# Kernel tuning notes

Measured on AMD Instinct MI355X. Metric: run time of the kernel, lower is better.

The kernel has to match this reference:

```python
import jax, jax.numpy as jnp
import numpy as np
from jax import lax

B, C, H, W = 32, 512, 56, 56
CO = 512
EPS = 1e-5

def binarize(x):
    # sign binarization with hardtanh straight-through estimator (BNN 1w1a)
    xc = jnp.clip(x, -1.0, 1.0)
    return xc + lax.stop_gradient(jnp.sign(x) - xc)

def batchnorm(y, g, b, m, v):
    # inference-mode BN with running stats, per-channel over NCHW
    inv = g * lax.rsqrt(v + EPS)
    return y * inv[None, :, None, None] + (b - m * inv)[None, :, None, None]

def setup_inputs() -> dict:
    key = jax.random.key(0)
    ks = jax.random.split(key, 11)
    return {
        "x": jax.random.normal(ks[0], (B, C, H, W), dtype=jnp.float32),
        "w_dw": jax.random.normal(ks[1], (C, 1, 3, 3), dtype=jnp.float32),
        "w_pw": jax.random.normal(ks[2], (CO, C, 1, 1), dtype=jnp.float32),
        "g1": jax.random.uniform(ks[3], (C,), dtype=jnp.float32),
        "b1": jax.random.normal(ks[4], (C,), dtype=jnp.float32),
        "m1": jax.random.normal(ks[5], (C,), dtype=jnp.float32),
        "v1": jax.random.uniform(ks[6], (C,), dtype=jnp.float32),
        "g2": jax.random.uniform(ks[7], (CO,), dtype=jnp.float32),
        "b2": jax.random.normal(ks[8], (CO,), dtype=jnp.float32),
        "m2": jax.random.normal(ks[9], (CO,), dtype=jnp.float32),
        "v2": jax.random.uniform(ks[10], (CO,), dtype=jnp.float32),
    }

def reference(x, w_dw, w_pw, g1, b1, m1, v1, g2, b2, m2, v2):
    dn = ('NCHW', 'OIHW', 'NCHW')
    # binary depthwise 3x3, stride 1, pad 1, groups=C
    out = lax.conv_general_dilated(
        binarize(x), binarize(w_dw), window_strides=(1, 1),
        padding=((1, 1), (1, 1)), feature_group_count=C,
        dimension_numbers=dn)
    out = batchnorm(out, g1, b1, m1, v1)
    # binary pointwise 1x1
    out = lax.conv_general_dilated(
        binarize(out), binarize(w_pw), window_strides=(1, 1),
        padding=((0, 0), (0, 0)), dimension_numbers=dn)
    out = batchnorm(out, g2, b2, m2, v2)
    return out
```

## Files before the change

### kernel.cpp

```cpp
#include <hip/hip_runtime.h>

#define BB 32
#define CC 512
#define COO 512
#define HH 56
#define WW 56
#define HW 3136
#define NPOS 100352
#define EPSF 1e-5f

typedef unsigned long long u64;
typedef unsigned int u32;
typedef unsigned short u16;
typedef float f32x4 __attribute__((ext_vector_type(4)));

#define OFF_S1      0
#define OFF_WBITS   6422528
#define OFF_WN      6455296
#define OFF_NT      6455872
#define OFF_BN2INV  6456832
#define OFF_BN2BETA 6458880

__global__ __launch_bounds__(256) void setup_kernel(
    const float* __restrict__ w_dw, const float* __restrict__ w_pw,
    const float* __restrict__ g1, const float* __restrict__ b1,
    const float* __restrict__ m1, const float* __restrict__ v1,
    const float* __restrict__ g2, const float* __restrict__ b2,
    const float* __restrict__ m2, const float* __restrict__ v2,
    u64* __restrict__ wbits, u64* __restrict__ wn, u64* __restrict__ NT,
    float* __restrict__ bn2inv, float* __restrict__ bn2beta) {
    const int t = blockIdx.x * 256 + threadIdx.x;

    {
        int o = t >> 3, wi = t & 7;
        const float* wp = w_pw + (size_t)o * CC + wi * 64;
        u64 wrd = 0;
        #pragma unroll 8
        for (int k = 0; k < 64; ++k)
            wrd |= (u64)(wp[k] >= 0.f) << k;
        wbits[t] = wrd;
    }

    if (t < CC) {
        float i2 = g2[t] / sqrtf(v2[t] + EPSF);
        bn2inv[t]  = i2;
        bn2beta[t] = b2[t] - m2[t] * i2;
    } else if (t >= 512 && t < 584) {
        int q = t - 512, cw = q & 7, tap = q >> 3;
        u64 wv = 0;
        for (int cl = 0; cl < 64; ++cl)
            wv |= (u64)(w_dw[(size_t)(cw * 64 + cl) * 9 + tap] < 0.f) << cl;
        wn[tap * 8 + cw] = wv;
    } else if (t >= 1024 && t < 1048) {
        int q = t - 1024, cat = q / 8, cw = q % 8;
        const int Nv = (cat == 0) ? 9 : ((cat == 1) ? 6 : 4);
        u64 p0 = 0, p1 = 0, p2 = 0, p3 = 0, F = 0;
        for (int cl = 0; cl < 64; ++cl) {
            int c = cw * 64 + cl;
            float i1 = g1[c] / sqrtf(v1[c] + EPSF);
            float be = b1[c] - m1[c] * i1;
            int T, f;
            if (i1 > 0.f) {
                double h = ((double)Nv - (double)be / (double)i1) * 0.5;
                f = 0;
                if (!(h > 0.0)) T = 0;
                else if (h > 15.0) T = 15;
                else T = (int)ceil(h);
            } else if (i1 < 0.f) {
                double h = ((double)Nv - (double)be / (double)i1) * 0.5;
                f = 1;
                if (h < 0.0) T = 0;
                else if (h >= 15.0) T = 15;
                else { T = (int)floor(h) + 1; if (T > 15) T = 15; }
            } else {
                f = 0;
                T = (be >= 0.f) ? 0 : 15;
            }
            unsigned nt = (~(unsigned)T) & 0xFu;
            p0 |= (u64)(nt & 1) << cl;
            p1 |= (u64)((nt >> 1) & 1) << cl;
            p2 |= (u64)((nt >> 2) & 1) << cl;
            p3 |= (u64)((nt >> 3) & 1) << cl;
            F  |= (u64)f << cl;
        }
        u64* d = NT + (size_t)(cat * 8 + cw) * 5;
        d[0] = p0; d[1] = p1; d[2] = p2; d[3] = p3; d[4] = F;
    }
}

__device__ __forceinline__ void fa(u64 a, u64 b, u64 c, u64& s, u64& cy) {
    u64 ab = a ^ b;
    s  = ab ^ c;
    cy = (ab & c) | (a & b);
}

__global__ __launch_bounds__(256, 4) void dwfused_kernel(
    const float* __restrict__ x, const u64* __restrict__ wn,
    const u64* __restrict__ NT, u64* __restrict__ s1) {
    __shared__ u64 xb[16 * 56];
    const int strip = blockIdx.x;
    const int cw    = blockIdx.y;
    const int b     = blockIdx.z;
    const int tid   = threadIdx.x;
    const int r0    = strip * 14;

    const float* xc = x + ((size_t)b * CC + cw * 64) * HW;
    u16* xb16 = (u16*)xb;

    for (int tau = tid; tau < 896; tau += 256) {
        const int cg     = tau / 224;
        const int rem    = tau - cg * 224;
        const int lrow   = rem / 14;
        const int colgrp = rem - lrow * 14;
        const int h      = r0 - 1 + lrow;
        const int col0   = colgrp * 4;
        u16 o0 = 0, o1 = 0, o2 = 0, o3 = 0;
        if (h >= 0 && h < HH) {
            const float* bp = xc + (size_t)(cg * 16) * HW + h * WW + col0;
            f32x4 vv[16];
            #pragma unroll
            for (int cl = 0; cl < 16; ++cl)
                vv[cl] = __builtin_nontemporal_load((const f32x4*)(bp + (size_t)cl * HW));
            u32 a0 = 0, a1 = 0, a2 = 0, a3 = 0;
            #pragma unroll
            for (int cl = 0; cl < 16; ++cl) {
                a0 |= (__float_as_uint(vv[cl].x) >> 31) << cl;
                a1 |= (__float_as_uint(vv[cl].y) >> 31) << cl;
                a2 |= (__float_as_uint(vv[cl].z) >> 31) << cl;
                a3 |= (__float_as_uint(vv[cl].w) >> 31) << cl;
            }
            o0 = (u16)(~a0); o1 = (u16)(~a1); o2 = (u16)(~a2); o3 = (u16)(~a3);
        }
        const int wbase = lrow * 56 + col0;
        xb16[(wbase + 0) * 4 + cg] = o0;
        xb16[(wbase + 1) * 4 + cg] = o1;
        xb16[(wbase + 2) * 4 + cg] = o2;
        xb16[(wbase + 3) * 4 + cg] = o3;
    }
    __syncthreads();

    if (tid >= 196) return;
    const int q      = tid / 14;
    const int colgrp = tid - q * 14;
    const int col0   = colgrp * 4;
    const int r      = r0 + q;
    const int lrow   = q + 1;

    const int c_m1 = (col0 == 0)  ? 0  : col0 - 1;
    const int c_p4 = (col0 == 52) ? 55 : col0 + 4;

    const u64* rowT = xb + (lrow - 1) * 56;
    const u64* rowM = xb + lrow * 56;
    const u64* rowB = xb + (lrow + 1) * 56;

    u64 rT[6], rM[6], rB[6];
    rT[0] = rowT[c_m1]; rT[1] = rowT[col0];   rT[2] = rowT[col0+1];
    rT[3] = rowT[col0+2]; rT[4] = rowT[col0+3]; rT[5] = rowT[c_p4];
    rM[0] = rowM[c_m1]; rM[1] = rowM[col0];   rM[2] = rowM[col0+1];
    rM[3] = rowM[col0+2]; rM[4] = rowM[col0+3]; rM[5] = rowM[c_p4];
    rB[0] = rowB[c_m1]; rB[1] = rowB[col0];   rB[2] = rowB[col0+1];
    rB[3] = rowB[col0+2]; rB[4] = rowB[col0+3]; rB[5] = rowB[c_p4];

    const u64 w00 = wn[0*8+cw], w01 = wn[1*8+cw], w02 = wn[2*8+cw];
    const u64 w10 = wn[3*8+cw], w11 = wn[4*8+cw], w12 = wn[5*8+cw];
    const u64 w20 = wn[6*8+cw], w21 = wn[7*8+cw], w22 = wn[8*8+cw];

    const u64 mt = (r > 0)    ? ~0ull : 0ull;
    const u64 mb = (r < 55)   ? ~0ull : 0ull;
    const u64 mL = (col0 > 0) ? ~0ull : 0ull;
    const u64 mR = (col0 < 52)? ~0ull : 0ull;

    const bool rowe = (r == 0) || (r == 55);
    const u64* NTc = NT + (size_t)cw * 5;
    u64 A0 = rowe ? NTc[40+0] : NTc[0];
    u64 A1 = rowe ? NTc[40+1] : NTc[1];
    u64 A2 = rowe ? NTc[40+2] : NTc[2];
    u64 A3 = rowe ? NTc[40+3] : NTc[3];
    u64 A4 = rowe ? NTc[40+4] : NTc[4];
    u64 B0 = rowe ? NTc[80+0] : NTc[40+0];
    u64 B1 = rowe ? NTc[80+1] : NTc[40+1];
    u64 B2 = rowe ? NTc[80+2] : NTc[40+2];
    u64 B3 = rowe ? NTc[80+3] : NTc[40+3];
    u64 B4 = rowe ? NTc[80+4] : NTc[40+4];

    u64 out[4];
    #pragma unroll
    for (int j = 0; j < 4; ++j) {
        u64 e0 = (rT[j]   ^ w00) & mt;
        u64 e1 = (rT[j+1] ^ w01) & mt;
        u64 e2 = (rT[j+2] ^ w02) & mt;
        u64 e3 = (rM[j]   ^ w10);
        u64 e4 = (rM[j+1] ^ w11);
        u64 e5 = (rM[j+2] ^ w12);
        u64 e6 = (rB[j]   ^ w20) & mb;
        u64 e7 = (rB[j+1] ^ w21) & mb;
        u64 e8 = (rB[j+2] ^ w22) & mb;
        if (j == 0) { e0 &= mL; e3 &= mL; e6 &= mL; }
        if (j == 3) { e2 &= mR; e5 &= mR; e8 &= mR; }

        u64 sa, ca, sb, cb, sc, cc, E0, cd, se, ce;
        fa(e0, e1, e2, sa, ca);
        fa(e3, e4, e5, sb, cb);
        fa(e6, e7, e8, sc, cc);
        fa(sa, sb, sc, E0, cd);
        fa(ca, cb, cc, se, ce);
        u64 E1 = se ^ cd, cf = se & cd;
        u64 E2 = ce ^ cf, E3 = ce & cf;

        u64 n0, n1, n2, n3, Fv;
        if (j == 0) {
            u64 m = (col0 == 0) ? ~0ull : 0ull;
            n0 = (B0 & m) | (A0 & ~m); n1 = (B1 & m) | (A1 & ~m);
            n2 = (B2 & m) | (A2 & ~m); n3 = (B3 & m) | (A3 & ~m);
            Fv = (B4 & m) | (A4 & ~m);
        } else if (j == 3) {
            u64 m = (col0 == 52) ? ~0ull : 0ull;
            n0 = (B0 & m) | (A0 & ~m); n1 = (B1 & m) | (A1 & ~m);
            n2 = (B2 & m) | (A2 & ~m); n3 = (B3 & m) | (A3 & ~m);
            Fv = (B4 & m) | (A4 & ~m);
        } else {
            n0 = A0; n1 = A1; n2 = A2; n3 = A3; Fv = A4;
        }

        u64 c = E0 | n0;
        c = (E1 & n1) | (c & (E1 | n1));
        c = (E2 & n2) | (c & (E2 | n2));
        c = (E3 & n3) | (c & (E3 | n3));
        out[j] = c ^ Fv;
    }

    u64* sp = s1 + (size_t)cw * NPOS + (size_t)b * HW + r * WW + col0;
    *(ulonglong2*)(sp)     = make_ulonglong2(out[0], out[1]);
    *(ulonglong2*)(sp + 2) = make_ulonglong2(out[2], out[3]);
}

__global__ __launch_bounds__(256) void pw_kernel(
    const u64* __restrict__ s1, const u64* __restrict__ wbits,
    const float* __restrict__ bn2inv, const float* __restrict__ bn2beta,
    float* __restrict__ out) {
    __shared__ u64  wb[128 * 8];
    __shared__ float inv_s[128], beta_s[128];
    const int tid = threadIdx.x;
    const int o0  = blockIdx.y * 128;

    for (int i = tid; i < 1024; i += 256) wb[i] = wbits[(size_t)o0 * 8 + i];
    if (tid < 128) { inv_s[tid] = bn2inv[o0 + tid]; beta_s[tid] = bn2beta[o0 + tid]; }
    __syncthreads();

    const size_t p   = (size_t)blockIdx.x * 256 + tid;
    const int    b   = (int)(p / HW);
    const int    idx = (int)(p - (size_t)b * HW);

    u64 r0 = __builtin_nontemporal_load(s1 + 0u * NPOS + p);
    u64 r1 = __builtin_nontemporal_load(s1 + 1u * NPOS + p);
    u64 r2 = __builtin_nontemporal_load(s1 + 2u * NPOS + p);
    u64 r3 = __builtin_nontemporal_load(s1 + 3u * NPOS + p);
    u64 r4 = __builtin_nontemporal_load(s1 + 4u * NPOS + p);
    u64 r5 = __builtin_nontemporal_load(s1 + 5u * NPOS + p);
    u64 r6 = __builtin_nontemporal_load(s1 + 6u * NPOS + p);
    u64 r7 = __builtin_nontemporal_load(s1 + 7u * NPOS + p);

    float* outp = out + ((size_t)b * COO) * HW + idx;

    for (int ol = 0; ol < 128; ++ol) {
        const u64* w8 = wb + ol * 8;
        int d = __popcll(r0 ^ w8[0]) + __popcll(r1 ^ w8[1])
              + __popcll(r2 ^ w8[2]) + __popcll(r3 ^ w8[3])
              + __popcll(r4 ^ w8[4]) + __popcll(r5 ^ w8[5])
              + __popcll(r6 ^ w8[6]) + __popcll(r7 ^ w8[7]);
        float res = (float)(CC - 2 * d);
        __builtin_nontemporal_store(fmaf(res, inv_s[ol], beta_s[ol]),
                                    outp + (size_t)(o0 + ol) * HW);
    }
}

extern "C" void kernel_launch(void* const* d_in, const int* in_sizes, int n_in,
                              void* d_out, int out_size, void* d_ws, size_t ws_size,
                              hipStream_t stream) {
    const float* x    = (const float*)d_in[0];
    const float* w_dw = (const float*)d_in[1];
    const float* w_pw = (const float*)d_in[2];
    const float* g1   = (const float*)d_in[3];
    const float* b1   = (const float*)d_in[4];
    const float* m1   = (const float*)d_in[5];
    const float* v1   = (const float*)d_in[6];
    const float* g2   = (const float*)d_in[7];
    const float* b2   = (const float*)d_in[8];
    const float* m2   = (const float*)d_in[9];
    const float* v2   = (const float*)d_in[10];

    char* ws = (char*)d_ws;
    u64*   s1      = (u64*)(ws + OFF_S1);
    u64*   wbits   = (u64*)(ws + OFF_WBITS);
    u64*   wn      = (u64*)(ws + OFF_WN);
    u64*   NTarr   = (u64*)(ws + OFF_NT);
    float* bn2inv  = (float*)(ws + OFF_BN2INV);
    float* bn2beta = (float*)(ws + OFF_BN2BETA);

    setup_kernel<<<16, 256, 0, stream>>>(w_dw, w_pw, g1, b1, m1, v1, g2, b2, m2, v2,
                                         wbits, wn, NTarr, bn2inv, bn2beta);

    dim3 gf(4, 8, BB);
    dwfused_kernel<<<gf, 256, 0, stream>>>(x, wn, NTarr, s1);

    dim3 g2d(392, 4);
    pw_kernel<<<g2d, 256, 0, stream>>>(s1, wbits, bn2inv, bn2beta, (float*)d_out);
}
```

Baseline: 133.2 us.

## Compute four positions per thread in pointwise kernel with vectorized loads and stores

The pointwise binary conv kernel now gives each thread four consecutive spatial positions and splits the 128 output channels of a block across the four waves, 32 each. Each weight row read from shared memory is reused across four positions, and outputs are written as 16-byte float4 stores instead of scalar stores. The cost is that each wave reloads the same 64x4 activation words, so activation traffic from global/L2 rises fourfold per block, and register pressure goes up. Because HW=3136 is divisible by 4, a group of four positions never straddles a batch boundary.

```diff
diff --git a/kernel.cpp b/kernel.cpp
--- a/kernel.cpp
+++ b/kernel.cpp
@@ -13,6 +13,7 @@
 typedef unsigned int u32;
 typedef unsigned short u16;
 typedef float f32x4 __attribute__((ext_vector_type(4)));
+typedef unsigned long long u64x2 __attribute__((ext_vector_type(2)));
 
 #define OFF_S1      0
 #define OFF_WBITS   6422528
@@ -247,30 +248,56 @@
     if (tid < 128) { inv_s[tid] = bn2inv[o0 + tid]; beta_s[tid] = bn2beta[o0 + tid]; }
     __syncthreads();
 
-    const size_t p   = (size_t)blockIdx.x * 256 + tid;
+    const int lane = tid & 63;
+    const int wv   = tid >> 6;
+    const size_t p = (size_t)blockIdx.x * 256 + (size_t)lane * 4;
     const int    b   = (int)(p / HW);
     const int    idx = (int)(p - (size_t)b * HW);
 
-    u64 r0 = __builtin_nontemporal_load(s1 + 0u * NPOS + p);
-    u64 r1 = __builtin_nontemporal_load(s1 + 1u * NPOS + p);
-    u64 r2 = __builtin_nontemporal_load(s1 + 2u * NPOS + p);
-    u64 r3 = __builtin_nontemporal_load(s1 + 3u * NPOS + p);
-    u64 r4 = __builtin_nontemporal_load(s1 + 4u * NPOS + p);
-    u64 r5 = __builtin_nontemporal_load(s1 + 5u * NPOS + p);
-    u64 r6 = __builtin_nontemporal_load(s1 + 6u * NPOS + p);
-    u64 r7 = __builtin_nontemporal_load(s1 + 7u * NPOS + p);
+    u64 r0[4], r1[4], r2[4], r3[4], r4[4], r5[4], r6[4], r7[4];
+    #pragma unroll
+    for (int h = 0; h < 1; ++h) {}
+    {
+        const u64* sp;
+        u64x2 qa, qb;
+        sp = s1 + 0u * NPOS + p; qa = __builtin_nontemporal_load((const u64x2*)sp); qb = __builtin_nontemporal_load((const u64x2*)(sp + 2));
+        r0[0] = qa.x; r0[1] = qa.y; r0[2] = qb.x; r0[3] = qb.y;
+        sp = s1 + 1u * NPOS + p; qa = __builtin_nontemporal_load((const u64x2*)sp); qb = __builtin_nontemporal_load((const u64x2*)(sp + 2));
+        r1[0] = qa.x; r1[1] = qa.y; r1[2] = qb.x; r1[3] = qb.y;
+        sp = s1 + 2u * NPOS + p; qa = __builtin_nontemporal_load((const u64x2*)sp); qb = __builtin_nontemporal_load((const u64x2*)(sp + 2));
+        r2[0] = qa.x; r2[1] = qa.y; r2[2] = qb.x; r2[3] = qb.y;
+        sp = s1 + 3u * NPOS + p; qa = __builtin_nontemporal_load((const u64x2*)sp); qb = __builtin_nontemporal_load((const u64x2*)(sp + 2));
+        r3[0] = qa.x; r3[1] = qa.y; r3[2] = qb.x; r3[3] = qb.y;
+        sp = s1 + 4u * NPOS + p; qa = __builtin_nontemporal_load((const u64x2*)sp); qb = __builtin_nontemporal_load((const u64x2*)(sp + 2));
+        r4[0] = qa.x; r4[1] = qa.y; r4[2] = qb.x; r4[3] = qb.y;
+        sp = s1 + 5u * NPOS + p; qa = __builtin_nontemporal_load((const u64x2*)sp); qb = __builtin_nontemporal_load((const u64x2*)(sp + 2));
+        r5[0] = qa.x; r5[1] = qa.y; r5[2] = qb.x; r5[3] = qb.y;
+        sp = s1 + 6u * NPOS + p; qa = __builtin_nontemporal_load((const u64x2*)sp); qb = __builtin_nontemporal_load((const u64x2*)(sp + 2));
+        r6[0] = qa.x; r6[1] = qa.y; r6[2] = qb.x; r6[3] = qb.y;
+        sp = s1 + 7u * NPOS + p; qa = __builtin_nontemporal_load((const u64x2*)sp); qb = __builtin_nontemporal_load((const u64x2*)(sp + 2));
+        r7[0] = qa.x; r7[1] = qa.y; r7[2] = qb.x; r7[3] = qb.y;
+    }
 
     float* outp = out + ((size_t)b * COO) * HW + idx;
-
-    for (int ol = 0; ol < 128; ++ol) {
-        const u64* w8 = wb + ol * 8;
-        int d = __popcll(r0 ^ w8[0]) + __popcll(r1 ^ w8[1])
-              + __popcll(r2 ^ w8[2]) + __popcll(r3 ^ w8[3])
-              + __popcll(r4 ^ w8[4]) + __popcll(r5 ^ w8[5])
-              + __popcll(r6 ^ w8[6]) + __popcll(r7 ^ w8[7]);
-        float res = (float)(CC - 2 * d);
-        __builtin_nontemporal_store(fmaf(res, inv_s[ol], beta_s[ol]),
-                                    outp + (size_t)(o0 + ol) * HW);
+    const int olbase = wv * 32;
+
+    #pragma unroll 4
+    for (int ol = 0; ol < 32; ++ol) {
+        const int o = olbase + ol;
+        const u64* w8 = wb + o * 8;
+        const u64 q0 = w8[0], q1 = w8[1], q2 = w8[2], q3 = w8[3];
+        const u64 q4 = w8[4], q5 = w8[5], q6 = w8[6], q7 = w8[7];
+        const float iv = inv_s[o], bt = beta_s[o];
+        f32x4 res;
+        #pragma unroll
+        for (int j = 0; j < 4; ++j) {
+            int d = __popcll(r0[j] ^ q0) + __popcll(r1[j] ^ q1)
+                  + __popcll(r2[j] ^ q2) + __popcll(r3[j] ^ q3)
+                  + __popcll(r4[j] ^ q4) + __popcll(r5[j] ^ q5)
+                  + __popcll(r6[j] ^ q6) + __popcll(r7[j] ^ q7);
+            res[j] = fmaf((float)(CC - 2 * d), iv, bt);
+        }
+        __builtin_nontemporal_store(res, (f32x4*)(outp + (size_t)(o0 + o) * HW));
     }
 }
 
```

Result: slower. 145.1 us (+8.9%).
